# Kernel tuning notes

Measured on AMD Instinct MI355X. Metric: run time of the kernel, lower is better.

## Reference

```python
import jax, jax.numpy as jnp
import numpy as np

N, E, IN, HID, OUT = 50000, 800000, 128, 128, 4
EPS = 1e-16  # PyG softmax denominator epsilon


def setup_inputs() -> dict:
    key = jax.random.key(0)
    ks = jax.random.split(key, 12)
    g = lambda k, shp, fan: jax.random.normal(k, shp, jnp.float32) * (1.0 / np.sqrt(fan))
    return {
        "x": jax.random.normal(ks[0], (N, IN), jnp.float32),
        "edge_index": jax.random.randint(ks[1], (2, E), 0, N),
        "W1": g(ks[2], (IN, HID), IN),
        "att_l1": g(ks[3], (HID,), HID),
        "att_r1": g(ks[4], (HID,), HID),
        "b1": jnp.zeros((HID,), jnp.float32),
        "W2": g(ks[5], (HID, HID), HID),
        "att_l2": g(ks[6], (HID,), HID),
        "att_r2": g(ks[7], (HID,), HID),
        "b2": jnp.zeros((HID,), jnp.float32),
        "Wc": g(ks[8], (2 * HID, OUT), 2 * HID),
        "bc": jnp.zeros((OUT,), jnp.float32),
    }


def supergat_layer(x, src, dst, W, att_l, att_r, b, n_nodes):
    """SuperGATConv, attention_type='MX', heads=1, concat, eval mode (no dropout)."""
    h = x @ W                                   # [N, C] linear transform (no bias)
    hj, hi = h[src], h[dst]                     # gather source / target feats per edge [E', C]
    logits = jnp.sum(hi * hj, axis=-1)          # MX dot-product logits [E']
    alpha = hj @ att_l + hi @ att_r             # GAT-style additive score [E']
    alpha = alpha * jax.nn.sigmoid(logits)      # MX gating
    # segment softmax over destination node
    amax = jax.ops.segment_max(alpha, dst, num_segments=n_nodes)
    ea = jnp.exp(alpha - amax[dst])
    denom = jax.ops.segment_sum(ea, dst, num_segments=n_nodes)
    w = ea / (denom[dst] + EPS)
    # scatter-aggregate weighted messages
    out = jax.ops.segment_sum(hj * w[:, None], dst, num_segments=n_nodes)
    return out + b


def reference(x, edge_index, W1, att_l1, att_r1, b1, W2, att_l2, att_r2, b2, Wc, bc):
    row, col = edge_index[0], edge_index[1]
    loop = jnp.arange(N)
    src = jnp.concatenate([row, loop])          # add self-loops (PyG default)
    dst = jnp.concatenate([col, loop])
    h = supergat_layer(x, src, dst, W1, att_l1, att_r1, b1, N)
    h = jax.nn.relu(h)
    h = supergat_layer(h, src, dst, W2, att_l2, att_r2, b2, N)
    edge_emb = jnp.concatenate([h[row], h[col]], axis=-1)  # [E, 2*HID]
    return edge_emb @ Wc + bc                    # [E, OUT]
```

## Files before the change

kernel.cpp:

```cpp
#include <hip/hip_runtime.h>
#include <hip/hip_fp16.h>
#include <math.h>

#define C 128
#define EPSV 1e-16f
#define BCAP 64

typedef _Float16 half2v __attribute__((ext_vector_type(2)));
typedef _Float16 half8v __attribute__((ext_vector_type(8)));
typedef float float4v __attribute__((ext_vector_type(4)));

__device__ __forceinline__ float fdot2(half2v a, half2v b, float c) {
#if __has_builtin(__builtin_amdgcn_fdot2)
    return __builtin_amdgcn_fdot2(a, b, c, false);
#else
    return c + (float)a.x * (float)b.x + (float)a.y * (float)b.y;
#endif
}

__device__ __forceinline__ float fastrcp(float x) {
#if __has_builtin(__builtin_amdgcn_rcpf)
    return __builtin_amdgcn_rcpf(x);
#else
    return 1.0f / x;
#endif
}

__device__ __forceinline__ void unpack8(uint4 a, uint4 b, half2v* h) {
    h[0] = __builtin_bit_cast(half2v, a.x);
    h[1] = __builtin_bit_cast(half2v, a.y);
    h[2] = __builtin_bit_cast(half2v, a.z);
    h[3] = __builtin_bit_cast(half2v, a.w);
    h[4] = __builtin_bit_cast(half2v, b.x);
    h[5] = __builtin_bit_cast(half2v, b.y);
    h[6] = __builtin_bit_cast(half2v, b.z);
    h[7] = __builtin_bit_cast(half2v, b.w);
}


__global__ __launch_bounds__(256) void zero_kernel(int* __restrict__ p, int n) {
    int i = blockIdx.x * 256 + threadIdx.x;
    if (i < n) p[i] = 0;
}

__global__ __launch_bounds__(256) void fill_kernel(const int* __restrict__ rowA, const int* __restrict__ colA,
                                                   int* __restrict__ cursor, int* __restrict__ bucket, int e) {
    int i = blockIdx.x * 256 + threadIdx.x;
    if (i < e) {
        int c = colA[i];
        int p = atomicAdd(&cursor[c], 1);
        if (p < BCAP) bucket[c * BCAP + p] = rowA[i];
    }
}


template <bool SRC16>
__global__ __launch_bounds__(256) void gemm_att_mfma(const void* __restrict__ Asrc, const float* __restrict__ W,
                                                     const float* __restrict__ attl, const float* __restrict__ attr,
                                                     __half* __restrict__ Hh, float* __restrict__ al,
                                                     float* __restrict__ ar, int M) {
    __shared__ __half Ah[64][136];
    __shared__ __half Wt[128][136];

    int t = threadIdx.x;
    int lane = t & 63;
    int w = t >> 6;
    int quad = lane >> 4;
    int n16 = lane & 15;
    int row0 = blockIdx.x * 64;

    {
        int k = t >> 1;
        int cbase = (t & 1) * 64;
        const float4* Wr = (const float4*)(W + (size_t)k * C + cbase);
        #pragma unroll
        for (int q = 0; q < 16; q++) {
            float4 wv = Wr[q];
            int c = cbase + q * 4;
            Wt[c][k]     = __float2half(wv.x);
            Wt[c + 1][k] = __float2half(wv.y);
            Wt[c + 2][k] = __float2half(wv.z);
            Wt[c + 3][k] = __float2half(wv.w);
        }
    }
    {
        int r = t >> 2;
        int ks = (t & 3) * 32;
        int gr = row0 + r;
        if (SRC16) {
            const uint4* src = (const uint4*)((const __half*)Asrc + (size_t)gr * C + ks);
            uint4 z = make_uint4(0, 0, 0, 0);
            #pragma unroll
            for (int q = 0; q < 4; q++) {
                uint4 v = (gr < M) ? src[q] : z;
                *(uint4*)&Ah[r][ks + q * 8] = v;
            }
        } else {
            const float4* src = (const float4*)((const float*)Asrc + (size_t)gr * C + ks);
            #pragma unroll
            for (int q = 0; q < 8; q++) {
                float4 v = (gr < M) ? src[q] : make_float4(0.f, 0.f, 0.f, 0.f);
                __half2 lo = __floats2half2_rn(v.x, v.y);
                __half2 hi2 = __floats2half2_rn(v.z, v.w);
                uint2 pk;
                pk.x = *(unsigned int*)&lo;
                pk.y = *(unsigned int*)&hi2;
                *(uint2*)&Ah[r][ks + q * 4] = pk;
            }
        }
    }
    __syncthreads();

    float4v acc[8];
    #pragma unroll
    for (int ct = 0; ct < 8; ct++) acc[ct] = (float4v){0.f, 0.f, 0.f, 0.f};
    int mrow = w * 16 + n16;
    #pragma unroll
    for (int ks = 0; ks < 4; ks++) {
        int k0 = ks * 32 + quad * 8;
        half8v a = *(half8v*)&Ah[mrow][k0];
        #pragma unroll
        for (int ct = 0; ct < 8; ct++) {
            half8v b = *(half8v*)&Wt[ct * 16 + n16][k0];
            acc[ct] = __builtin_amdgcn_mfma_f32_16x16x32_f16(a, b, acc[ct], 0, 0, 0);
        }
    }

    __syncthreads();
    #pragma unroll
    for (int ct = 0; ct < 8; ct++) {
        #pragma unroll
        for (int r = 0; r < 4; r++) {
            Ah[w * 16 + quad * 4 + r][ct * 16 + n16] = __float2half(acc[ct][r]);
        }
    }
    __syncthreads();

    {
        int r = t >> 2;
        int seg = (t & 3) * 32;
        int gr = row0 + r;
        uint4 d[4];
        #pragma unroll
        for (int q = 0; q < 4; q++) d[q] = *(uint4*)&Ah[r][seg + q * 8];
        float pl = 0.f, pr = 0.f;
        #pragma unroll
        for (int q = 0; q < 4; q++) {
            half2v hv[4];
            hv[0] = __builtin_bit_cast(half2v, d[q].x);
            hv[1] = __builtin_bit_cast(half2v, d[q].y);
            hv[2] = __builtin_bit_cast(half2v, d[q].z);
            hv[3] = __builtin_bit_cast(half2v, d[q].w);
            #pragma unroll
            for (int j = 0; j < 4; j++) {
                float2 f = make_float2((float)hv[j].x, (float)hv[j].y);
                int c = seg + q * 8 + j * 2;
                pl += f.x * attl[c] + f.y * attl[c + 1];
                pr += f.x * attr[c] + f.y * attr[c + 1];
            }
        }
        if (gr < M) {
            uint4* dst = (uint4*)&Hh[(size_t)gr * C + seg];
            #pragma unroll
            for (int q = 0; q < 4; q++) dst[q] = d[q];
        }
        pl += __shfl_xor(pl, 1);
        pl += __shfl_xor(pl, 2);
        pr += __shfl_xor(pr, 1);
        pr += __shfl_xor(pr, 2);
        if ((t & 3) == 0 && gr < M) { al[gr] = pl; ar[gr] = pr; }
    }
}


__device__ __forceinline__ float2 agg_core8(const __half* __restrict__ Hh, const int* __restrict__ bucket,
                                            const int* __restrict__ cnt, const float* __restrict__ al,
                                            const float* __restrict__ ar, const float* __restrict__ bvec,
                                            int node, int lane, float* __restrict__ mb) {
    int sub = lane >> 3;
    int k = lane & 7;

    int deg = cnt[node];
    uint4 ha = *(const uint4*)&Hh[(size_t)node * C + 8 * k];
    uint4 hb = *(const uint4*)&Hh[(size_t)node * C + 64 + 8 * k];
    float aln = al[node];
    float arn = ar[node];
    if (deg > BCAP) deg = BCAP;
    int base = node * BCAP;

    int myI = sub + 8 * k;
    int myS = 0;
    float myAls = 0.f;
    if (myI < deg) myS = bucket[base + myI];
    if (myI < deg) myAls = al[myS];

    int i = sub;
    int srcLane = sub * 8;
    uint4 ra = {}, rb = {};
    float cal0 = 0.f;
    if (i < deg) {
        int s = __shfl(myS, srcLane);
        cal0 = __shfl(myAls, srcLane);
        ra = *(const uint4*)&Hh[(size_t)s * C + 8 * k];
        rb = *(const uint4*)&Hh[(size_t)s * C + 64 + 8 * k];
    }

    half2v hi[8];
    unpack8(ha, hb, hi);
    float ds = 0.f;
    #pragma unroll
    for (int j = 0; j < 8; j++) ds = fdot2(hi[j], hi[j], ds);
    ds += __shfl_xor(ds, 1);
    ds += __shfl_xor(ds, 2);
    ds += __shfl_xor(ds, 4);
    float pself = __expf((aln + arn) * fastrcp(1.0f + __expf(-ds)));

    bool s0 = (sub == 0);
    float denom = s0 ? pself : 0.0f;
    float acc[16];
    #pragma unroll
    for (int j = 0; j < 8; j++) {
        acc[2 * j]     = s0 ? pself * (float)hi[j].x : 0.0f;
        acc[2 * j + 1] = s0 ? pself * (float)hi[j].y : 0.0f;
    }

    while (i < deg) {
        uint4 ca = ra, cb = rb;
        float cal = cal0;
        int inext = i + 8;
        if (inext < deg) {
            int s = __shfl(myS, srcLane + 1);
            cal0 = __shfl(myAls, srcLane + 1);
            ra = *(const uint4*)&Hh[(size_t)s * C + 8 * k];
            rb = *(const uint4*)&Hh[(size_t)s * C + 64 + 8 * k];
        }
        half2v hj[8];
        unpack8(ca, cb, hj);
        float d = 0.f;
        #pragma unroll
        for (int j = 0; j < 8; j++) d = fdot2(hi[j], hj[j], d);
        d += __shfl_xor(d, 1);
        d += __shfl_xor(d, 2);
        d += __shfl_xor(d, 4);
        float p = __expf((cal + arn) * fastrcp(1.0f + __expf(-d)));
        denom += p;
        #pragma unroll
        for (int j = 0; j < 8; j++) {
            acc[2 * j]     += p * (float)hj[j].x;
            acc[2 * j + 1] += p * (float)hj[j].y;
        }
        i = inext;
        srcLane++;
    }

    denom += __shfl_xor(denom, 8);
    denom += __shfl_xor(denom, 16);
    denom += __shfl_xor(denom, 32);

    float* myrow = mb + lane * 20;
    *(float4*)(myrow)      = make_float4(acc[0], acc[1], acc[2], acc[3]);
    *(float4*)(myrow + 4)  = make_float4(acc[4], acc[5], acc[6], acc[7]);
    *(float4*)(myrow + 8)  = make_float4(acc[8], acc[9], acc[10], acc[11]);
    *(float4*)(myrow + 12) = make_float4(acc[12], acc[13], acc[14], acc[15]);

    int pr = lane;
    int kk = (pr < 32) ? (pr >> 2) : ((pr - 32) >> 2);
    int jj = (pr < 32) ? (pr & 3) : (4 + ((pr - 32) & 3));
    float sx = 0.f, sy = 0.f;
    #pragma unroll
    for (int s = 0; s < 8; s++) {
        float2 v = *(const float2*)(mb + (s * 8 + kk) * 20 + 2 * jj);
        sx += v.x;
        sy += v.y;
    }

    float inv = fastrcp(denom + EPSV);
    float2 bv = *(const float2*)&bvec[2 * lane];
    return make_float2(sx * inv + bv.x, sy * inv + bv.y);
}

__global__ __launch_bounds__(256) void agg_kernel(const __half* __restrict__ Hh, const int* __restrict__ bucket,
                                                  const int* __restrict__ cnt, const float* __restrict__ al,
                                                  const float* __restrict__ ar, const float* __restrict__ bvec,
                                                  __half* __restrict__ O, int n) {
    __shared__ __align__(16) float mergeBuf[4][64 * 20];
    int w = threadIdx.x >> 6;
    int node = blockIdx.x * 4 + w;
    int lane = threadIdx.x & 63;
    if (node >= n) return;
    float2 o2 = agg_core8(Hh, bucket, cnt, al, ar, bvec, node, lane, &mergeBuf[w][0]);
    __half2 hv = __floats2half2_rn(fmaxf(o2.x, 0.f), fmaxf(o2.y, 0.f));
    *(unsigned int*)&O[(size_t)node * C + 2 * lane] = *(unsigned int*)&hv;
}

__global__ __launch_bounds__(256) void agg_proj_kernel(const __half* __restrict__ Hh, const int* __restrict__ bucket,
                                                       const int* __restrict__ cnt, const float* __restrict__ al,
                                                       const float* __restrict__ ar, const float* __restrict__ bvec,
                                                       const float* __restrict__ Wc, float* __restrict__ P1,
                                                       float* __restrict__ P2, int n) {
    __shared__ __align__(16) float mergeBuf[4][64 * 20];
    __shared__ __align__(16) float poutBuf[4][128];
    int w = threadIdx.x >> 6;
    int node = blockIdx.x * 4 + w;
    int lane = threadIdx.x & 63;
    if (node >= n) return;
    float2 o2 = agg_core8(Hh, bucket, cnt, al, ar, bvec, node, lane, &mergeBuf[w][0]);

    float* pout = &poutBuf[w][0];
    *(float2*)&pout[2 * lane] = o2;
    int o = lane & 7;
    int grp = lane >> 3;
    int table = o >> 2;
    int dim = o & 3;
    const float* wc = Wc + ((size_t)(table * C + grp * 16)) * 4 + dim;
    float s = 0.f;
    #pragma unroll
    for (int q = 0; q < 4; q++) {
        int qq = (q + grp) & 3;
        float4 v = *(const float4*)&pout[grp * 16 + qq * 4];
        s += v.x * wc[(qq * 4 + 0) * 4] + v.y * wc[(qq * 4 + 1) * 4]
           + v.z * wc[(qq * 4 + 2) * 4] + v.w * wc[(qq * 4 + 3) * 4];
    }
    s += __shfl_xor(s, 8);
    s += __shfl_xor(s, 16);
    s += __shfl_xor(s, 32);
    if (lane < 8) {
        if (table == 0) P1[(size_t)node * 4 + dim] = s;
        else            P2[(size_t)node * 4 + dim] = s;
    }
}

__global__ __launch_bounds__(256) void edge_out_kernel(const float4* __restrict__ P1, const float4* __restrict__ P2,
                                                       const int* __restrict__ rowA, const int* __restrict__ colA,
                                                       const float* __restrict__ bc, float4* __restrict__ out, int e) {
    int i = blockIdx.x * 256 + threadIdx.x;
    if (i >= e) return;
    float4 a = P1[rowA[i]];
    float4 b = P2[colA[i]];
    float4 bcv = *(const float4*)bc;
    out[i] = make_float4(a.x + b.x + bcv.x, a.y + b.y + bcv.y, a.z + b.z + bcv.z, a.w + b.w + bcv.w);
}


extern "C" void kernel_launch(void* const* d_in, const int* in_sizes, int n_in,
                              void* d_out, int out_size, void* d_ws, size_t ws_size,
                              hipStream_t stream) {
    const float* x     = (const float*)d_in[0];
    const int*   ei    = (const int*)d_in[1];
    const float* W1    = (const float*)d_in[2];
    const float* attl1 = (const float*)d_in[3];
    const float* attr1 = (const float*)d_in[4];
    const float* b1    = (const float*)d_in[5];
    const float* W2    = (const float*)d_in[6];
    const float* attl2 = (const float*)d_in[7];
    const float* attr2 = (const float*)d_in[8];
    const float* b2    = (const float*)d_in[9];
    const float* Wc    = (const float*)d_in[10];
    const float* bc    = (const float*)d_in[11];
    float* out = (float*)d_out;

    const int N = in_sizes[0] / C;
    const int E = in_sizes[1] / 2;
    const int* rowA = ei;
    const int* colA = ei + E;

    __half* Hh     = (__half*)d_ws;
    __half* G2in   = Hh + (size_t)N * C;
    float*  al     = (float*)(G2in + (size_t)N * C);
    float*  ar     = al + N;
    int*    cursor = (int*)(ar + N);
    int*    bucket = cursor + N;
    float*  P1     = (float*)(bucket + (size_t)N * BCAP);
    float*  P2     = P1 + (size_t)N * 4;

    const int nbN = (N + 255) / 256;
    const int nbE = (E + 255) / 256;
    const int gemmBlocks = (N + 63) / 64;
    const int nodeBlocks = (N + 3) / 4;

    zero_kernel<<<nbN, 256, 0, stream>>>(cursor, N);
    fill_kernel<<<nbE, 256, 0, stream>>>(rowA, colA, cursor, bucket, E);

    gemm_att_mfma<false><<<gemmBlocks, 256, 0, stream>>>(x, W1, attl1, attr1, Hh, al, ar, N);
    agg_kernel<<<nodeBlocks, 256, 0, stream>>>(Hh, bucket, cursor, al, ar, b1, G2in, N);

    gemm_att_mfma<true><<<gemmBlocks, 256, 0, stream>>>(G2in, W2, attl2, attr2, Hh, al, ar, N);
    agg_proj_kernel<<<nodeBlocks, 256, 0, stream>>>(Hh, bucket, cursor, al, ar, b2, Wc, P1, P2, N);

    edge_out_kernel<<<nbE, 256, 0, stream>>>((const float4*)P1, (const float4*)P2, rowA, colA, bc, (float4*)out, E);
}
```

Baseline: 279.2 us.

## Use 16-bit bucket indices and pre-convert x and W to fp16

Stores neighbor indices in the bucket as unsigned short instead of int, which halves the bucket memory traffic in fill and aggregation. Node ids up to 50000 fit in 16 bits, but this breaks for graphs with more than 65535 nodes. Also adds separate kernels that convert x to fp16 and pre-transpose W1/W2 to fp16 once. The GEMM then loads ready fp16 tiles with coalesced uint4 copies instead of converting and transposing per block. This adds an extra pass over x and two more launches.

```diff
diff --git a/kernel.cpp b/kernel.cpp
--- a/kernel.cpp
+++ b/kernel.cpp
@@ -44,18 +44,47 @@
 }
 
 __global__ __launch_bounds__(256) void fill_kernel(const int* __restrict__ rowA, const int* __restrict__ colA,
-                                                   int* __restrict__ cursor, int* __restrict__ bucket, int e) {
+                                                   int* __restrict__ cursor, unsigned short* __restrict__ bucket,
+                                                   int e) {
     int i = blockIdx.x * 256 + threadIdx.x;
     if (i < e) {
         int c = colA[i];
         int p = atomicAdd(&cursor[c], 1);
-        if (p < BCAP) bucket[c * BCAP + p] = rowA[i];
-    }
-}
-
-
-template <bool SRC16>
-__global__ __launch_bounds__(256) void gemm_att_mfma(const void* __restrict__ Asrc, const float* __restrict__ W,
+        if (p < BCAP) bucket[c * BCAP + p] = (unsigned short)rowA[i];
+    }
+}
+
+
+__global__ __launch_bounds__(256) void convert_x_kernel(const float* __restrict__ x, __half* __restrict__ x16, int n8) {
+    int i = blockIdx.x * 256 + threadIdx.x;
+    if (i >= n8) return;
+    float4 a = ((const float4*)x)[2 * i];
+    float4 b = ((const float4*)x)[2 * i + 1];
+    __half2 h0 = __floats2half2_rn(a.x, a.y);
+    __half2 h1 = __floats2half2_rn(a.z, a.w);
+    __half2 h2 = __floats2half2_rn(b.x, b.y);
+    __half2 h3 = __floats2half2_rn(b.z, b.w);
+    uint4 pk;
+    pk.x = *(unsigned int*)&h0;
+    pk.y = *(unsigned int*)&h1;
+    pk.z = *(unsigned int*)&h2;
+    pk.w = *(unsigned int*)&h3;
+    ((uint4*)x16)[i] = pk;
+}
+
+__global__ __launch_bounds__(256) void prep_w_kernel(const float* __restrict__ W1, const float* __restrict__ W2,
+                                                     __half* __restrict__ Wt1, __half* __restrict__ Wt2) {
+    int id = blockIdx.x * 256 + threadIdx.x;
+    const float* W = (id < 16384) ? W1 : W2;
+    __half* Wt = (id < 16384) ? Wt1 : Wt2;
+    int e = id & 16383;
+    int c = e >> 7;
+    int k = e & 127;
+    Wt[c * C + k] = __float2half(W[(size_t)k * C + c]);
+}
+
+
+__global__ __launch_bounds__(256) void gemm_att_mfma(const __half* __restrict__ A16, const __half* __restrict__ WtG,
                                                      const float* __restrict__ attl, const float* __restrict__ attr,
                                                      __half* __restrict__ Hh, float* __restrict__ al,
                                                      float* __restrict__ ar, int M) {
@@ -69,45 +98,20 @@
     int n16 = lane & 15;
     int row0 = blockIdx.x * 64;
 
-    {
-        int k = t >> 1;
-        int cbase = (t & 1) * 64;
-        const float4* Wr = (const float4*)(W + (size_t)k * C + cbase);
-        #pragma unroll
-        for (int q = 0; q < 16; q++) {
-            float4 wv = Wr[q];
-            int c = cbase + q * 4;
-            Wt[c][k]     = __float2half(wv.x);
-            Wt[c + 1][k] = __float2half(wv.y);
-            Wt[c + 2][k] = __float2half(wv.z);
-            Wt[c + 3][k] = __float2half(wv.w);
-        }
-    }
-    {
-        int r = t >> 2;
-        int ks = (t & 3) * 32;
+    #pragma unroll
+    for (int q = 0; q < 8; q++) {
+        int idx = t + q * 256;
+        int c = idx >> 4, kq = idx & 15;
+        *(uint4*)&Wt[c][kq * 8] = ((const uint4*)&WtG[(size_t)c * C])[kq];
+    }
+    uint4 z = make_uint4(0, 0, 0, 0);
+    #pragma unroll
+    for (int q = 0; q < 4; q++) {
+        int idx = t + q * 256;
+        int r = idx >> 4, kq = idx & 15;
         int gr = row0 + r;
-        if (SRC16) {
-            const uint4* src = (const uint4*)((const __half*)Asrc + (size_t)gr * C + ks);
-            uint4 z = make_uint4(0, 0, 0, 0);
-            #pragma unroll
-            for (int q = 0; q < 4; q++) {
-                uint4 v = (gr < M) ? src[q] : z;
-                *(uint4*)&Ah[r][ks + q * 8] = v;
-            }
-        } else {
-            const float4* src = (const float4*)((const float*)Asrc + (size_t)gr * C + ks);
-            #pragma unroll
-            for (int q = 0; q < 8; q++) {
-                float4 v = (gr < M) ? src[q] : make_float4(0.f, 0.f, 0.f, 0.f);
-                __half2 lo = __floats2half2_rn(v.x, v.y);
-                __half2 hi2 = __floats2half2_rn(v.z, v.w);
-                uint2 pk;
-                pk.x = *(unsigned int*)&lo;
-                pk.y = *(unsigned int*)&hi2;
-                *(uint2*)&Ah[r][ks + q * 4] = pk;
-            }
-        }
+        uint4 v = (gr < M) ? ((const uint4*)&A16[(size_t)gr * C])[kq] : z;
+        *(uint4*)&Ah[r][kq * 8] = v;
     }
     __syncthreads();
 
@@ -173,7 +177,7 @@
 }
 
 
-__device__ __forceinline__ float2 agg_core8(const __half* __restrict__ Hh, const int* __restrict__ bucket,
+__device__ __forceinline__ float2 agg_core8(const __half* __restrict__ Hh, const unsigned short* __restrict__ bucket,
                                             const int* __restrict__ cnt, const float* __restrict__ al,
                                             const float* __restrict__ ar, const float* __restrict__ bvec,
                                             int node, int lane, float* __restrict__ mb) {
@@ -191,7 +195,7 @@
     int myI = sub + 8 * k;
     int myS = 0;
     float myAls = 0.f;
-    if (myI < deg) myS = bucket[base + myI];
+    if (myI < deg) myS = (int)bucket[base + myI];
     if (myI < deg) myAls = al[myS];
 
     int i = sub;
@@ -279,7 +283,7 @@
     return make_float2(sx * inv + bv.x, sy * inv + bv.y);
 }
 
-__global__ __launch_bounds__(256) void agg_kernel(const __half* __restrict__ Hh, const int* __restrict__ bucket,
+__global__ __launch_bounds__(256) void agg_kernel(const __half* __restrict__ Hh, const unsigned short* __restrict__ bucket,
                                                   const int* __restrict__ cnt, const float* __restrict__ al,
                                                   const float* __restrict__ ar, const float* __restrict__ bvec,
                                                   __half* __restrict__ O, int n) {
@@ -293,7 +297,7 @@
     *(unsigned int*)&O[(size_t)node * C + 2 * lane] = *(unsigned int*)&hv;
 }
 
-__global__ __launch_bounds__(256) void agg_proj_kernel(const __half* __restrict__ Hh, const int* __restrict__ bucket,
+__global__ __launch_bounds__(256) void agg_proj_kernel(const __half* __restrict__ Hh, const unsigned short* __restrict__ bucket,
                                                        const int* __restrict__ cnt, const float* __restrict__ al,
                                                        const float* __restrict__ ar, const float* __restrict__ bvec,
                                                        const float* __restrict__ Wc, float* __restrict__ P1,
@@ -366,10 +370,13 @@
 
     __half* Hh     = (__half*)d_ws;
     __half* G2in   = Hh + (size_t)N * C;
-    float*  al     = (float*)(G2in + (size_t)N * C);
+    __half* X16    = G2in + (size_t)N * C;
+    __half* Wt1    = X16 + (size_t)N * C;
+    __half* Wt2    = Wt1 + C * C;
+    float*  al     = (float*)(Wt2 + C * C);
     float*  ar     = al + N;
     int*    cursor = (int*)(ar + N);
-    int*    bucket = cursor + N;
+    unsigned short* bucket = (unsigned short*)(cursor + N);
     float*  P1     = (float*)(bucket + (size_t)N * BCAP);
     float*  P2     = P1 + (size_t)N * 4;
 
@@ -377,14 +384,17 @@
     const int nbE = (E + 255) / 256;
     const int gemmBlocks = (N + 63) / 64;
     const int nodeBlocks = (N + 3) / 4;
+    const int n8 = N * C / 8;
 
     zero_kernel<<<nbN, 256, 0, stream>>>(cursor, N);
     fill_kernel<<<nbE, 256, 0, stream>>>(rowA, colA, cursor, bucket, E);
-
-    gemm_att_mfma<false><<<gemmBlocks, 256, 0, stream>>>(x, W1, attl1, attr1, Hh, al, ar, N);
+    convert_x_kernel<<<(n8 + 255) / 256, 256, 0, stream>>>(x, X16, n8);
+    prep_w_kernel<<<128, 256, 0, stream>>>(W1, W2, Wt1, Wt2);
+
+    gemm_att_mfma<<<gemmBlocks, 256, 0, stream>>>(X16, Wt1, attl1, attr1, Hh, al, ar, N);
     agg_kernel<<<nodeBlocks, 256, 0, stream>>>(Hh, bucket, cursor, al, ar, b1, G2in, N);
 
-    gemm_att_mfma<true><<<gemmBlocks, 256, 0, stream>>>(G2in, W2, attl2, attr2, Hh, al, ar, N);
+    gemm_att_mfma<<<gemmBlocks, 256, 0, stream>>>(G2in, Wt2, attl2, attr2, Hh, al, ar, N);
     agg_proj_kernel<<<nodeBlocks, 256, 0, stream>>>(Hh, bucket, cursor, al, ar, b2, Wc, P1, P2, N);
 
     edge_out_kernel<<<nbE, 256, 0, stream>>>((const float4*)P1, (const float4*)P2, rowA, colA, bc, (float4*)out, E);
```

Result: faster. 272.3 us (-2.4%).
